# Kernel optimization log

Measured on AMD Instinct MI355X. Metric: run time of the kernel, lower is better.

## Reference

```python
import jax, jax.numpy as jnp
import numpy as np
from math import factorial, sqrt, pi

MUL = 8
LS = [0, 1, 2]                       # l values for both Rs_in and Rs_out
RS = [(MUL, l) for l in LS]
N_NODES = 20000
N_EDGES = 100000
FEAT = sum(m * (2 * l + 1) for m, l in RS)       # 72
R_TOT = sum(mo * mi * (2 * min(lo, li) + 1) for mo, lo in RS for mi, li in RS)  # 1216
L_MAX = max(LS) + max(LS)            # 4
RSH_DIM = (L_MAX + 1) ** 2           # 25
NB, H = 10, 100                      # radial basis size / hidden width
MIN_R, MAX_R = 0.7, 3.2
SWISH_SCALE = 1.679177               # e3nn rescaled swish factor


def _w3j_entry(j1, j2, j3, m1, m2, m3):
    # complex-basis Wigner 3j (Racah formula)
    if m1 + m2 + m3 != 0 or not (abs(j1 - j2) <= j3 <= j1 + j2):
        return 0.0
    t1, t2 = j2 - m1 - j3, j1 + m2 - j3
    kmin, kmax = max(0, t1, t2), min(j1 + j2 - j3, j1 - m1, j2 + m2)
    s = sum((-1) ** k / (factorial(k) * factorial(k - t1) * factorial(k - t2)
                         * factorial(j1 + j2 - j3 - k) * factorial(j1 - m1 - k) * factorial(j2 + m2 - k))
            for k in range(kmin, kmax + 1))
    pref = (-1) ** (j1 - j2 - m3) * sqrt(
        factorial(j1 + j2 - j3) * factorial(j1 - j2 + j3) * factorial(-j1 + j2 + j3) / factorial(j1 + j2 + j3 + 1)
        * factorial(j1 + m1) * factorial(j1 - m1) * factorial(j2 + m2) * factorial(j2 - m2)
        * factorial(j3 + m3) * factorial(j3 - m3))
    return pref * s


def _real_cob(l):
    # complex->real spherical-harmonic change of basis
    U = np.zeros((2 * l + 1, 2 * l + 1), dtype=complex)
    U[l, l] = 1.0
    s = 1.0 / np.sqrt(2.0)
    for m in range(1, l + 1):
        U[l + m, l + m] = (-1) ** m * s
        U[l + m, l - m] = s
        U[l - m, l - m] = 1j * s
        U[l - m, l + m] = -1j * ((-1) ** m) * s
    return U


def _wigner3j_real(l1, l2, l3):
    w = np.zeros((2 * l1 + 1, 2 * l2 + 1, 2 * l3 + 1))
    for m1 in range(-l1, l1 + 1):
        for m2 in range(-l2, l2 + 1):
            m3 = -m1 - m2
            if abs(m3) <= l3:
                w[m1 + l1, m2 + l2, m3 + l3] = _w3j_entry(l1, l2, l3, m1, m2, m3)
    T = np.einsum('am,bn,cp,mnp->abc', _real_cob(l1), _real_cob(l2), _real_cob(l3), w.astype(complex))
    C = T.real if np.linalg.norm(T.real) >= np.linalg.norm(T.imag) else T.imag
    n = np.linalg.norm(C)
    return (C / n if n > 0 else C).astype(np.float32)


# precomputed constants (coupling coefficients + normalization), as in MinimalNetwork.__init__
C3 = {(lo, li, lf): jnp.asarray(_wigner3j_real(lo, li, lf))
      for _, lo in RS for _, li in RS for lf in range(abs(lo - li), lo + li + 1)}


def _norm_coef():
    nc = np.zeros((len(RS), len(RS)), dtype=np.float32)
    for i, (_, lo) in enumerate(RS):
        num = sum(mi * (2 * min(lo, li) + 1) for mi, li in RS)
        nc[i, :] = sqrt(4 * pi) * sqrt(2 * lo + 1) / sqrt(num)
    return jnp.asarray(nc)

NORM = _norm_coef()


def _swish(x):
    return SWISH_SCALE * x * jax.nn.sigmoid(x)


def _radial(r, Ws):
    # GaussianRadialModel: gaussian basis -> 3 hidden swish layers -> linear out
    centers = jnp.linspace(MIN_R, MAX_R, NB)
    sigma = (MAX_R - MIN_R) / (NB - 1)
    x = jnp.exp(-(((r[:, None] - centers) / sigma) ** 2))
    for W in Ws[:-1]:
        x = _swish(x @ (W / jnp.sqrt(jnp.asarray(W.shape[0], x.dtype))))
    W = Ws[-1]
    return x @ (W / jnp.sqrt(jnp.asarray(W.shape[0], x.dtype)))


def _tensor_message(F_src, rsh, R):
    # F_src: [E, FEAT] gathered source features; rsh: [E, 25]; R: [E, R_TOT]
    E = F_src.shape[0]
    f_offs = np.cumsum([0] + [m * (2 * l + 1) for m, l in RS])
    msgs, r_off = [], 0
    for i, (U, lo) in enumerate(RS):
        acc = jnp.zeros((E, U, 2 * lo + 1), F_src.dtype)
        for j, (V, li) in enumerate(RS):
            nlf = 2 * min(lo, li) + 1
            Rb = R[:, r_off:r_off + U * V * nlf].reshape(E, U, V, nlf)
            r_off += U * V * nlf
            Fb = F_src[:, f_offs[j]:f_offs[j + 1]].reshape(E, V, 2 * li + 1)
            for fi, lf in enumerate(range(abs(lo - li), lo + li + 1)):
                # K[e,mo,mi] = sum_mf C3[mo,mi,mf] * Y_lf[e,mf]
                K = jnp.einsum('oif,ef->eoi', C3[(lo, li, lf)], rsh[:, lf * lf:(lf + 1) * (lf + 1)])
                acc = acc + NORM[i, j] * jnp.einsum('eoi,evi,euv->euo', K, Fb, Rb[..., fi])
        msgs.append(acc.reshape(E, -1))
    return jnp.concatenate(msgs, axis=-1)


def _forward(features, edge_index, radii, rsh, Ws):
    R = _radial(radii, Ws)                                     # [E, R_TOT]
    msg = _tensor_message(features[edge_index[0]], rsh, R)     # [E, FEAT]
    # scatter-add aggregation at target nodes (MessagePassing aggr='add')
    return jnp.zeros((features.shape[0], msg.shape[1]), msg.dtype).at[edge_index[1]].add(msg)


def setup_inputs() -> dict:
    key = jax.random.key(0)
    ks = jax.random.split(key, 8)
    features = jax.random.normal(ks[0], (N_NODES, FEAT), jnp.float32)
    edge_index = jax.random.randint(ks[1], (2, N_EDGES), 0, N_NODES)
    radii = MIN_R + (MAX_R - MIN_R) * jax.random.uniform(ks[2], (N_EDGES,), jnp.float32)
    rsh = jax.random.normal(ks[3], (N_EDGES, RSH_DIM), jnp.float32)
    W0 = jax.random.normal(ks[4], (NB, H), jnp.float32)
    W1 = jax.random.normal(ks[5], (H, H), jnp.float32)
    W2 = jax.random.normal(ks[6], (H, H), jnp.float32)
    W3 = jax.random.normal(ks[7], (H, R_TOT), jnp.float32)
    return {"features": features, "edge_index": edge_index, "radii": radii, "rsh": rsh,
            "W0": W0, "W1": W1, "W2": W2, "W3": W3}


def reference(features, edge_index, radii, rsh, W0, W1, W2, W3):
    return _forward(features, edge_index, radii, rsh, (W0, W1, W2, W3))
```

## Files before the change

kernel.cpp:

```cpp
#include <hip/hip_runtime.h>
#include <hip/hip_bf16.h>
#include <math.h>


#define FEATD 72
#define NCOL 1216
#define SWISH_SCALE 1.679177f

typedef __attribute__((ext_vector_type(8))) short bf16x8;
typedef __attribute__((ext_vector_type(4))) float f32x4;

constexpr int NCOMBO = 19;
constexpr int CB_LO[NCOMBO] = {0,0,0,1,1,1,1,1,1,1,2,2,2,2,2,2,2,2,2};
constexpr int CB_LI[NCOMBO] = {0,1,2,0,1,1,1,2,2,2,0,1,1,1,2,2,2,2,2};
constexpr int CB_LF[NCOMBO] = {0,1,2,1,0,1,2,1,2,3,2,1,2,3,0,1,2,3,4};
constexpr int CB_OFF[NCOMBO] = {0,1,10,35,44,53,80,125,170,245,350,375,420,495,600,625,700,825,1000};
constexpr int CB_SZ[NCOMBO]  = {1,9,25,9,9,27,45,45,75,105,25,45,75,105,25,75,125,175,225};
constexpr int C3TOT = 1225;

constexpr int C3OFFT[3][3][5] = {
  { {0,-1,-1,-1,-1}, {-1,1,-1,-1,-1}, {-1,-1,10,-1,-1} },
  { {-1,35,-1,-1,-1}, {44,53,80,-1,-1}, {-1,125,170,245,-1} },
  { {-1,-1,350,-1,-1}, {-1,375,420,495,-1}, {600,625,700,825,1000} }
};
constexpr int ROFFT[3][3] = {{0,64,128},{192,256,448},{640,704,896}};
constexpr int FOFFT[3]   = {0,8,32};

__device__ const double d_fact[11] = {1.,1.,2.,6.,24.,120.,720.,5040.,40320.,362880.,3628800.};

__device__ double w3j_entry(int j1,int j2,int j3,int m1,int m2,int m3){
  if (m1+m2+m3 != 0) return 0.0;
  int dj = j1-j2; if (dj<0) dj=-dj;
  if (j3 < dj || j3 > j1+j2) return 0.0;
  int t1 = j2 - m1 - j3, t2 = j1 + m2 - j3;
  int kmin = 0; if (t1>kmin) kmin=t1; if (t2>kmin) kmin=t2;
  int kmax = j1+j2-j3; if (j1-m1<kmax) kmax=j1-m1; if (j2+m2<kmax) kmax=j2+m2;
  double s = 0.0;
  for (int k=kmin;k<=kmax;++k){
    double den = d_fact[k]*d_fact[k-t1]*d_fact[k-t2]*d_fact[j1+j2-j3-k]
               * d_fact[j1-m1-k]*d_fact[j2+m2-k];
    s += ((k&1)? -1.0:1.0)/den;
  }
  double pref = sqrt(d_fact[j1+j2-j3]*d_fact[j1-j2+j3]*d_fact[-j1+j2+j3]/d_fact[j1+j2+j3+1]
               * d_fact[j1+m1]*d_fact[j1-m1]*d_fact[j2+m2]*d_fact[j2-m2]
               * d_fact[j3+m3]*d_fact[j3-m3]);
  int ex = j1-j2-m3;
  if (ex & 1) pref = -pref;
  return pref*s;
}

__device__ void cob(int l, int r, int c, double& re, double& im){
  re = 0.0; im = 0.0;
  int mr = r - l, mc = c - l;
  const double s = 0.70710678118654752440;
  if (mr == 0) { if (mc == 0) re = 1.0; return; }
  if (mr > 0) {
    if (mc == mr)       re = (mr & 1) ? -s : s;
    else if (mc == -mr) re = s;
  } else {
    int m = -mr;
    if (mc == -m)      im = s;
    else if (mc == m)  im = (m & 1) ? s : -s;
  }
}

__global__ void c3_combined_kernel(float* __restrict__ C3f){
  __shared__ double sre[225], sim[225];
  const int c = blockIdx.x;
  const int lo = CB_LO[c], li = CB_LI[c], lf = CB_LF[c];
  const int off = CB_OFF[c], sz = CB_SZ[c];
  const int n2 = 2*li+1, n3 = 2*lf+1;
  const int t = threadIdx.x;

  for (int p=t; p<sz; p+=64){
    int a = p/(n2*n3), b = (p/n3)%n2, g = p%n3;
    double re=0.0, im=0.0;
    for (int m1=-lo; m1<=lo; ++m1){
      for (int m2=-li; m2<=li; ++m2){
        int m3 = -m1-m2;
        if (m3 < -lf || m3 > lf) continue;
        double w = w3j_entry(lo,li,lf,m1,m2,m3);
        if (w == 0.0) continue;
        double r1,i1,r2,i2,r3,i3;
        cob(lo, a, m1+lo, r1,i1);
        cob(li, b, m2+li, r2,i2);
        cob(lf, g, m3+lf, r3,i3);
        double rr = r1*r2 - i1*i2, ri = r1*i2 + i1*r2;
        double fr = rr*r3 - ri*i3, fi = rr*i3 + ri*r3;
        re += fr*w; im += fi*w;
      }
    }
    sre[p] = re; sim[p] = im;
  }
  __syncthreads();
  double s2r=0.0, s2i=0.0;
  for (int p=t; p<sz; p+=64){ double x=sre[p], y=sim[p]; s2r+=x*x; s2i+=y*y; }
  for (int m=1; m<64; m<<=1){ s2r += __shfl_xor(s2r, m, 64); s2i += __shfl_xor(s2i, m, 64); }
  bool useRe = (s2r >= s2i);
  double n = sqrt(useRe ? s2r : s2i);
  double inv = (n > 0.0) ? 1.0/n : 1.0;
  for (int p=t; p<sz; p+=64){
    double v = useRe ? sre[p] : sim[p];
    C3f[off+p] = (float)(v*inv);
  }
}

__global__ __launch_bounds__(256) void prep_combined_kernel(
    const float* __restrict__ W3, const float* __restrict__ W1,
    const float* __restrict__ W2, __hip_bfloat16* __restrict__ W3t,
    __hip_bfloat16* __restrict__ W1t, __hip_bfloat16* __restrict__ W2t)
{
  int idx = blockIdx.x*256 + threadIdx.x;
  constexpr int NW3 = 1216*128;
  constexpr int HALF = 112*128;
  if (idx < NW3){
    int cp = idx >> 7, k = idx & 127;
    int chunk = cp >> 6, r = cp & 63;
    int lo = CB_LO[chunk], li = CB_LI[chunk], lf = CB_LF[chunk];
    int lmin = lo<li ? lo : li;
    int nlf = 2*lmin+1;
    int fi = lf - (lo>li ? lo-li : li-lo);
    int c = ROFFT[lo][li] + r*nlf + fi;
    float v = (k < 100) ? 0.1f*W3[(size_t)k*NCOL + c] : 0.f;
    int swz = (r*16 + (k>>3)) ^ (r&7);
    W3t[(size_t)chunk*8192 + swz*8 + (k&7)] = __float2bfloat16(v);
  } else if (idx < NW3 + 2*HALF){
    int r2 = idx - NW3;
    const float* W = (r2 < HALF) ? W1 : W2;
    __hip_bfloat16* Wt = (r2 < HALF) ? W1t : W2t;
    int r = (r2 < HALF) ? r2 : r2 - HALF;
    int o = r >> 7, k = r & 127;
    float v = (o < 100 && k < 100) ? 0.1f*W[k*100+o] : 0.f;
    int swz = (o*16 + (k>>3)) ^ (o&7);
    Wt[swz*8 + (k&7)] = __float2bfloat16(v);
  }
}

constexpr int OF_W   = 0;
constexpr int OF_RT  = 16384;
constexpr int OF_ACC = 33792;
constexpr int OF_F   = 44032;
constexpr int OF_KV  = 63488;
constexpr int OF_C3  = 76288;
constexpr int OF_SRC = 81188;
constexpr int OF_TGT = 81444;
constexpr int SMEM_SZ = 81700;

constexpr int OF_RW   = 0;
constexpr int OF_BAS  = 28672;
constexpr int OF_HA   = 31232;
constexpr int OF_HB   = 48640;

__device__ __forceinline__ float swishf(float s){
  return SWISH_SCALE * s / (1.f + __expf(-s));
}

__device__ __forceinline__ void stage_w(const __hip_bfloat16* __restrict__ Wt,
                                        char* sW, int t)
{
  const int lane = t & 63, wv = t >> 6;
  const char* g = (const char*)Wt;
  #pragma unroll
  for (int i=0; i<7; ++i){
    const char* gsrc = g + (i*256 + wv*64 + lane)*16;
    __builtin_amdgcn_global_load_lds(
        (const __attribute__((address_space(1))) unsigned int*)gsrc,
        (__attribute__((address_space(3))) unsigned int*)(sW + i*4096 + wv*1024),
        16, 0, 0);
  }
}

__device__ __forceinline__ void radial_layer_lds(
    const __hip_bfloat16* __restrict__ sIn,
    const char* __restrict__ sW,
    __hip_bfloat16* __restrict__ sOut,
    int wv, int lr, int lq)
{
  bf16x8 bf[4];
  #pragma unroll
  for (int ks=0; ks<4; ++ks)
    bf[ks] = *(const bf16x8*)&sIn[(wv*16+lr)*136 + ks*32 + lq*8];
  f32x4 acc[7] = {};
  #pragma unroll
  for (int ks=0; ks<4; ++ks)
    #pragma unroll
    for (int ot=0; ot<7; ++ot){
      const int row = ot*16 + lr;
      const int u = (row*16 + ks*4 + lq) ^ (row & 7);
      bf16x8 a = *(const bf16x8*)(sW + u*16);
      acc[ot] = __builtin_amdgcn_mfma_f32_16x16x32_bf16(a, bf[ks], acc[ot], 0, 0, 0);
    }
  #pragma unroll
  for (int ot=0; ot<7; ++ot){
    __hip_bfloat16 hv[4];
    #pragma unroll
    for (int r=0; r<4; ++r)
      hv[r] = __float2bfloat16(swishf(acc[ot][r]));
    *(short4*)&sOut[(wv*16+lr)*136 + ot*16 + lq*4] = *(short4*)hv;
  }
  {
    int lane = lq*16 + lr;
    int row = lane & 15, q = lane >> 4;
    short4 z = {0,0,0,0};
    *(short4*)&sOut[(wv*16+row)*136 + 112 + q*4] = z;
  }
}

__device__ __forceinline__ void stage_chunk(const __hip_bfloat16* __restrict__ W3t,
                                            int chunk, char* sW, int t)
{
  const int lane = t & 63, wv = t >> 6;
  const char* g = (const char*)W3t + (size_t)chunk*16384;
  #pragma unroll
  for (int r=0; r<4; ++r){
    const char* gsrc = g + (wv*256 + r*64 + lane)*16;
    __builtin_amdgcn_global_load_lds(
        (const __attribute__((address_space(1))) unsigned int*)gsrc,
        (__attribute__((address_space(3))) unsigned int*)(sW + wv*4096 + r*1024),
        16, 0, 0);
  }
}

template<int LO,int LI,int LF>
__device__ __forceinline__ void kv_sec(float* kvb, const float* sC3,
                                       const float* __restrict__ rshrow,
                                       int e, int role)
{
  constexpr int NO = 2*LO+1, NI = 2*LI+1, NF = 2*LF+1;
  constexpr int C3B = C3OFFT[LO][LI][LF];
  float y[NF];
  #pragma unroll
  for (int mf=0; mf<NF; ++mf) y[mf] = rshrow[LF*LF + mf];
  for (int it = role; it < NO*NI; it += 4){
    float s = 0.f;
    #pragma unroll
    for (int mf=0; mf<NF; ++mf) s += sC3[C3B + it*NF + mf] * y[mf];
    kvb[e*25 + it] = s;
  }
}

template<int LO,int LI>
__device__ __forceinline__ void consume_sec(
    const float* sRt, const float* sFf, const float* kvb, float* sAcc,
    int e, int role)
{
  constexpr int NO = 2*LO+1, NI = 2*LI+1;
  constexpr int FO = FOFFT[LI];
  float H[2][NI];
  #pragma unroll
  for (int du=0; du<2; ++du)
    #pragma unroll
    for (int mi=0; mi<NI; ++mi) H[du][mi] = 0.f;

  #pragma unroll
  for (int vg=0; vg<2; ++vg){
    float fb[4*NI];
    #pragma unroll
    for (int p=0; p<NI; ++p)
      *(f32x4*)&fb[p*4] = *(const f32x4*)&sFf[e*76 + FO + vg*4*NI + p*4];
    #pragma unroll
    for (int du=0; du<2; ++du){
      const int u = role*2 + du;
      f32x4 rv = *(const f32x4*)&sRt[e*68 + u*8 + vg*4];
      #pragma unroll
      for (int v=0; v<4; ++v)
        #pragma unroll
        for (int mi=0; mi<NI; ++mi)
          H[du][mi] += rv[v] * fb[v*NI + mi];
    }
  }
  const int u0 = role*2, u1 = role*2 + 1;
  const int b0 = e*40 + ((LO==0) ? u0 : (LO==1) ? u0*3 : u0*5);
  const int b1 = e*40 + ((LO==0) ? u1 : (LO==1) ? u1*3 : u1*5);
  #pragma unroll
  for (int o=0; o<NO; ++o){
    float s0 = 0.f, s1 = 0.f;
    #pragma unroll
    for (int mi=0; mi<NI; ++mi){
      float kvv = kvb[e*25 + o*NI + mi];
      s0 += kvv * H[0][mi];
      s1 += kvv * H[1][mi];
    }
    sAcc[b0 + o] += s0;
    sAcc[b1 + o] += s1;
  }
}

__device__ __forceinline__ void mfma_sec(const char* sW, float* sRt,
                                         const bf16x8 (&hf)[4],
                                         int wv, int lr, int lq)
{
  f32x4 a4[4] = {};
  #pragma unroll
  for (int ks=0; ks<4; ++ks){
    #pragma unroll
    for (int ct=0; ct<4; ++ct){
      const int row = ct*16 + lr;
      const int u   = (row*16 + (ks*4 + lq)) ^ (row & 7);
      bf16x8 a = *(const bf16x8*)(sW + u*16);
      a4[ct] = __builtin_amdgcn_mfma_f32_16x16x32_bf16(a, hf[ks], a4[ct], 0, 0, 0);
    }
  }
  #pragma unroll
  for (int ct=0; ct<4; ++ct)
    *(f32x4*)&sRt[(wv*16 + lr)*68 + ct*16 + lq*4] = a4[ct];
}

template<int J0,int W>
__device__ __forceinline__ void flush_group(float* sAcc, float* __restrict__ out,
                                            const int* sTgt, int eb, int t,
                                            float nrm, int E)
{
  const int lane = t & 63, wv = t >> 6;
  __builtin_amdgcn_wave_barrier();
  for (int p = lane; p < 16*W; p += 64){
    int el = wv*16 + p/W, j = p%W;
    if (eb + el < E)
      atomicAdd(&out[(size_t)sTgt[el]*FEATD + J0 + j], nrm * sAcc[el*40 + j]);
    sAcc[el*40 + j] = 0.f;
  }
  __builtin_amdgcn_wave_barrier();
}

template<int LO,int LI,int LF,int PLO,int PLI,int PFLUSH,int CUR>
__device__ __forceinline__ void phase_pl(
    int chunk, const __hip_bfloat16* __restrict__ W3t, const bf16x8 (&hf)[4],
    char* sW, float* sRt, float* sFf, float* sKV, const float* sC3,
    const float* __restrict__ rshrow, float* sAcc,
    float* __restrict__ out, const int* sTgt, int eb, int t, int E)
{
  const int e = t >> 2, role = t & 3;
  const int lane = t & 63, wv = t >> 6;
  const int lr = lane & 15, lq = lane >> 4;

  __syncthreads();
  stage_chunk(W3t, chunk, sW, t);

  kv_sec<LO,LI,LF>(sKV + CUR*1600, sC3, rshrow, e, role);
  if constexpr (PLO >= 0)
    consume_sec<PLO,PLI>(sRt, sFf, sKV + (1-CUR)*1600, sAcc, e, role);
  if constexpr (PFLUSH == 0)
    flush_group<0,8>(sAcc, out, sTgt, eb, t, 0.72360125f, E);
  if constexpr (PFLUSH == 1)
    flush_group<8,24>(sAcc, out, sTgt, eb, t, 0.8204867f, E);

  __syncthreads();
  mfma_sec(sW, sRt, hf, wv, lr, lq);
  __builtin_amdgcn_wave_barrier();
}

__global__ __launch_bounds__(256,2) void fused_kernel(
    const float* __restrict__ feats, const int* __restrict__ ei,
    const float* __restrict__ radii, const float* __restrict__ rsh,
    const float* __restrict__ W0,
    const __hip_bfloat16* __restrict__ W1t, const __hip_bfloat16* __restrict__ W2t,
    const __hip_bfloat16* __restrict__ W3t, const float* __restrict__ C3g,
    float* __restrict__ out, int E)
{
  __shared__ __align__(16) char smem[SMEM_SZ];
  char*  sW   = smem + OF_W;
  float* sRt  = (float*)(smem + OF_RT);
  float* sAcc = (float*)(smem + OF_ACC);
  float* sFf  = (float*)(smem + OF_F);
  float* sKV  = (float*)(smem + OF_KV);
  float* sC3  = (float*)(smem + OF_C3);
  int*   sSrc = (int*)(smem + OF_SRC);
  int*   sTgt = (int*)(smem + OF_TGT);
  char*  sWr  = smem + OF_RW;
  float* sbas = (float*)(smem + OF_BAS);
  __hip_bfloat16* hA = (__hip_bfloat16*)(smem + OF_HA);
  __hip_bfloat16* hB = (__hip_bfloat16*)(smem + OF_HB);

  const int t = threadIdx.x;
  const int eb = blockIdx.x*64;
  const int lane = t & 63, wv = t >> 6;
  const int lr = lane & 15, lq = lane >> 4;

  stage_w(W1t, sWr, t);

  for (int p=t; p<640; p+=256){
    int er = p/10, k = p%10;
    int eg = eb + er;
    float r = (eg < E) ? radii[eg] : 0.f;
    float c = 0.7f + (2.5f/9.0f)*(float)k;
    float d = (r - c) * (9.0f/2.5f);
    sbas[p] = __expf(-d*d);
  }
  __syncthreads();
  for (int p=t; p<6400; p+=256){
    int er = p/100, o = p%100;
    float s = 0.f;
    #pragma unroll
    for (int k=0;k<10;++k) s += sbas[er*10+k]*W0[k*100+o];
    hA[er*136+o] = __float2bfloat16(swishf(s*0.3162277660168379f));
  }
  for (int p=t; p<64*36; p+=256){
    int er = p/36, k = 100 + p%36;
    hA[er*136+k] = __float2bfloat16(0.f);
  }
  __syncthreads();

  radial_layer_lds(hA, sWr, hB, wv, lr, lq);
  __syncthreads();
  stage_w(W2t, sWr, t);
  __syncthreads();
  radial_layer_lds(hB, sWr, hA, wv, lr, lq);
  __builtin_amdgcn_wave_barrier();

  bf16x8 hf[4];
  #pragma unroll
  for (int ks=0; ks<4; ++ks)
    hf[ks] = *(const bf16x8*)&hA[(wv*16+lr)*136 + ks*32 + lq*8];

  __syncthreads();

  for (int p=t; p<2560; p+=256) sAcc[p] = 0.f;
  for (int p=t; p<64; p+=256){
    int e = eb + p;
    sSrc[p] = (e < E) ? ei[e] : 0;
    sTgt[p] = (e < E) ? ei[E + e] : 0;
  }
  for (int p=t; p<C3TOT; p+=256) sC3[p] = C3g[p];
  __syncthreads();
  for (int p=t; p<64*72; p+=256){
    int el = p/72, j = p%72;
    sFf[el*76 + j] = feats[(size_t)sSrc[el]*72 + j];
  }
  __syncthreads();

  int eg = eb + (t >> 2); if (eg > E-1) eg = E-1;
  const float* rshrow = rsh + (size_t)eg*25;

  phase_pl<0,0,0, -1,-1, -1, 0>( 0, W3t, hf, sW, sRt, sFf, sKV, sC3, rshrow, sAcc, out, sTgt, eb, t, E);
  phase_pl<0,1,1,  0, 0, -1, 1>( 1, W3t, hf, sW, sRt, sFf, sKV, sC3, rshrow, sAcc, out, sTgt, eb, t, E);
  phase_pl<0,2,2,  0, 1, -1, 0>( 2, W3t, hf, sW, sRt, sFf, sKV, sC3, rshrow, sAcc, out, sTgt, eb, t, E);
  phase_pl<1,0,1,  0, 2,  0, 1>( 3, W3t, hf, sW, sRt, sFf, sKV, sC3, rshrow, sAcc, out, sTgt, eb, t, E);
  phase_pl<1,1,0,  1, 0, -1, 0>( 4, W3t, hf, sW, sRt, sFf, sKV, sC3, rshrow, sAcc, out, sTgt, eb, t, E);
  phase_pl<1,1,1,  1, 1, -1, 1>( 5, W3t, hf, sW, sRt, sFf, sKV, sC3, rshrow, sAcc, out, sTgt, eb, t, E);
  phase_pl<1,1,2,  1, 1, -1, 0>( 6, W3t, hf, sW, sRt, sFf, sKV, sC3, rshrow, sAcc, out, sTgt, eb, t, E);
  phase_pl<1,2,1,  1, 1, -1, 1>( 7, W3t, hf, sW, sRt, sFf, sKV, sC3, rshrow, sAcc, out, sTgt, eb, t, E);
  phase_pl<1,2,2,  1, 2, -1, 0>( 8, W3t, hf, sW, sRt, sFf, sKV, sC3, rshrow, sAcc, out, sTgt, eb, t, E);
  phase_pl<1,2,3,  1, 2, -1, 1>( 9, W3t, hf, sW, sRt, sFf, sKV, sC3, rshrow, sAcc, out, sTgt, eb, t, E);
  phase_pl<2,0,2,  1, 2,  1, 0>(10, W3t, hf, sW, sRt, sFf, sKV, sC3, rshrow, sAcc, out, sTgt, eb, t, E);
  phase_pl<2,1,1,  2, 0, -1, 1>(11, W3t, hf, sW, sRt, sFf, sKV, sC3, rshrow, sAcc, out, sTgt, eb, t, E);
  phase_pl<2,1,2,  2, 1, -1, 0>(12, W3t, hf, sW, sRt, sFf, sKV, sC3, rshrow, sAcc, out, sTgt, eb, t, E);
  phase_pl<2,1,3,  2, 1, -1, 1>(13, W3t, hf, sW, sRt, sFf, sKV, sC3, rshrow, sAcc, out, sTgt, eb, t, E);
  phase_pl<2,2,0,  2, 1, -1, 0>(14, W3t, hf, sW, sRt, sFf, sKV, sC3, rshrow, sAcc, out, sTgt, eb, t, E);
  phase_pl<2,2,1,  2, 2, -1, 1>(15, W3t, hf, sW, sRt, sFf, sKV, sC3, rshrow, sAcc, out, sTgt, eb, t, E);
  phase_pl<2,2,2,  2, 2, -1, 0>(16, W3t, hf, sW, sRt, sFf, sKV, sC3, rshrow, sAcc, out, sTgt, eb, t, E);
  phase_pl<2,2,3,  2, 2, -1, 1>(17, W3t, hf, sW, sRt, sFf, sKV, sC3, rshrow, sAcc, out, sTgt, eb, t, E);
  phase_pl<2,2,4,  2, 2, -1, 0>(18, W3t, hf, sW, sRt, sFf, sKV, sC3, rshrow, sAcc, out, sTgt, eb, t, E);

  {
    const int e = t >> 2, role = t & 3;
    consume_sec<2,2>(sRt, sFf, sKV + 0*1600, sAcc, e, role);
    flush_group<32,40>(sAcc, out, sTgt, eb, t, 0.9341652f, E);
  }
}

extern "C" void kernel_launch(void* const* d_in, const int* in_sizes, int n_in,
                              void* d_out, int out_size, void* d_ws, size_t ws_size,
                              hipStream_t stream)
{
  const float* feats = (const float*)d_in[0];
  const int*   ei    = (const int*)d_in[1];
  const float* radii = (const float*)d_in[2];
  const float* rsh   = (const float*)d_in[3];
  const float* W0    = (const float*)d_in[4];
  const float* W1    = (const float*)d_in[5];
  const float* W2    = (const float*)d_in[6];
  const float* W3    = (const float*)d_in[7];
  float* out = (float*)d_out;
  const int E = in_sizes[2];

  const int EPAD = ((E + 63)/64)*64;
  const int NBLK = EPAD/64;

  char* ws = (char*)d_ws;
  size_t off_b = 0;
  float*  C3f = (float*)(ws + off_b);  off_b += 8192;
  __hip_bfloat16* W3t = (__hip_bfloat16*)(ws + off_b); off_b += 335872;
  __hip_bfloat16* W1t = (__hip_bfloat16*)(ws + off_b); off_b += 30720;
  __hip_bfloat16* W2t = (__hip_bfloat16*)(ws + off_b); off_b += 30720;

  hipMemsetAsync(out, 0, (size_t)out_size*sizeof(float), stream);

  c3_combined_kernel<<<dim3(NCOMBO), dim3(64), 0, stream>>>(C3f);
  prep_combined_kernel<<<dim3((1216*128 + 2*112*128 + 255)/256), dim3(256), 0, stream>>>(
      W3, W1, W2, W3t, W1t, W2t);

  fused_kernel<<<dim3(NBLK), dim3(256), 0, stream>>>(
      feats, ei, radii, rsh, W0, W1t, W2t, W3t, C3f, out, E);
}
```

Baseline: 340.8 us.

## Read MFMA weight fragments directly from global memory instead of staging in LDS

```diff
diff --git a/kernel.cpp b/kernel.cpp
--- a/kernel.cpp
+++ b/kernel.cpp
@@ -111,70 +111,56 @@
     __hip_bfloat16* __restrict__ W1t, __hip_bfloat16* __restrict__ W2t)
 {
   int idx = blockIdx.x*256 + threadIdx.x;
-  constexpr int NW3 = 1216*128;
-  constexpr int HALF = 112*128;
+  constexpr int NW3 = 19*8192;
+  constexpr int HALF = 7*4*64*8;
   if (idx < NW3){
-    int cp = idx >> 7, k = idx & 127;
-    int chunk = cp >> 6, r = cp & 63;
+    int j = idx & 7, lane = (idx>>3)&63, kc = (idx>>9)&15, chunk = idx>>13;
+    int ks = kc & 3, ct = kc >> 2;
+    int r = ct*16 + (lane&15);
+    int k = ks*32 + (lane>>4)*8 + j;
     int lo = CB_LO[chunk], li = CB_LI[chunk], lf = CB_LF[chunk];
     int lmin = lo<li ? lo : li;
     int nlf = 2*lmin+1;
     int fi = lf - (lo>li ? lo-li : li-lo);
     int c = ROFFT[lo][li] + r*nlf + fi;
     float v = (k < 100) ? 0.1f*W3[(size_t)k*NCOL + c] : 0.f;
-    int swz = (r*16 + (k>>3)) ^ (r&7);
-    W3t[(size_t)chunk*8192 + swz*8 + (k&7)] = __float2bfloat16(v);
+    W3t[idx] = __float2bfloat16(v);
   } else if (idx < NW3 + 2*HALF){
     int r2 = idx - NW3;
     const float* W = (r2 < HALF) ? W1 : W2;
     __hip_bfloat16* Wt = (r2 < HALF) ? W1t : W2t;
     int r = (r2 < HALF) ? r2 : r2 - HALF;
-    int o = r >> 7, k = r & 127;
+    int j = r & 7, lane = (r>>3)&63, kc = r>>9;
+    int ks = kc & 3, ot = kc >> 2;
+    int o = ot*16 + (lane&15);
+    int k = ks*32 + (lane>>4)*8 + j;
     float v = (o < 100 && k < 100) ? 0.1f*W[k*100+o] : 0.f;
-    int swz = (o*16 + (k>>3)) ^ (o&7);
-    Wt[swz*8 + (k&7)] = __float2bfloat16(v);
-  }
-}
-
-constexpr int OF_W   = 0;
-constexpr int OF_RT  = 16384;
-constexpr int OF_ACC = 33792;
-constexpr int OF_F   = 44032;
-constexpr int OF_KV  = 63488;
-constexpr int OF_C3  = 76288;
-constexpr int OF_SRC = 81188;
-constexpr int OF_TGT = 81444;
-constexpr int SMEM_SZ = 81700;
-
-constexpr int OF_RW   = 0;
-constexpr int OF_BAS  = 28672;
-constexpr int OF_HA   = 31232;
-constexpr int OF_HB   = 48640;
+    Wt[r] = __float2bfloat16(v);
+  }
+}
+
+constexpr int OF_RT  = 0;
+constexpr int OF_ACC = 17408;
+constexpr int OF_F   = 27648;
+constexpr int OF_KV  = 47104;
+constexpr int OF_C3  = 53504;
+constexpr int OF_SRC = 58404;
+constexpr int OF_TGT = 58660;
+constexpr int SMEM_SZ = 58916;
+
+constexpr int OF_BAS  = 0;
+constexpr int OF_HA   = 2560;
+constexpr int OF_HB   = 19968;
 
 __device__ __forceinline__ float swishf(float s){
   return SWISH_SCALE * s / (1.f + __expf(-s));
 }
 
-__device__ __forceinline__ void stage_w(const __hip_bfloat16* __restrict__ Wt,
-                                        char* sW, int t)
-{
-  const int lane = t & 63, wv = t >> 6;
-  const char* g = (const char*)Wt;
-  #pragma unroll
-  for (int i=0; i<7; ++i){
-    const char* gsrc = g + (i*256 + wv*64 + lane)*16;
-    __builtin_amdgcn_global_load_lds(
-        (const __attribute__((address_space(1))) unsigned int*)gsrc,
-        (__attribute__((address_space(3))) unsigned int*)(sW + i*4096 + wv*1024),
-        16, 0, 0);
-  }
-}
-
-__device__ __forceinline__ void radial_layer_lds(
+__device__ __forceinline__ void radial_layer_glb(
     const __hip_bfloat16* __restrict__ sIn,
-    const char* __restrict__ sW,
+    const __hip_bfloat16* __restrict__ Wt,
     __hip_bfloat16* __restrict__ sOut,
-    int wv, int lr, int lq)
+    int lane, int wv, int lr, int lq)
 {
   bf16x8 bf[4];
   #pragma unroll
@@ -185,9 +171,7 @@
   for (int ks=0; ks<4; ++ks)
     #pragma unroll
     for (int ot=0; ot<7; ++ot){
-      const int row = ot*16 + lr;
-      const int u = (row*16 + ks*4 + lq) ^ (row & 7);
-      bf16x8 a = *(const bf16x8*)(sW + u*16);
+      bf16x8 a = *(const bf16x8*)&Wt[((ot*4+ks)*64 + lane)*8];
       acc[ot] = __builtin_amdgcn_mfma_f32_16x16x32_bf16(a, bf[ks], acc[ot], 0, 0, 0);
     }
   #pragma unroll
@@ -199,25 +183,10 @@
     *(short4*)&sOut[(wv*16+lr)*136 + ot*16 + lq*4] = *(short4*)hv;
   }
   {
-    int lane = lq*16 + lr;
-    int row = lane & 15, q = lane >> 4;
+    int l2 = lq*16 + lr;
+    int row = l2 & 15, q = l2 >> 4;
     short4 z = {0,0,0,0};
     *(short4*)&sOut[(wv*16+row)*136 + 112 + q*4] = z;
-  }
-}
-
-__device__ __forceinline__ void stage_chunk(const __hip_bfloat16* __restrict__ W3t,
-                                            int chunk, char* sW, int t)
-{
-  const int lane = t & 63, wv = t >> 6;
-  const char* g = (const char*)W3t + (size_t)chunk*16384;
-  #pragma unroll
-  for (int r=0; r<4; ++r){
-    const char* gsrc = g + (wv*256 + r*64 + lane)*16;
-    __builtin_amdgcn_global_load_lds(
-        (const __attribute__((address_space(1))) unsigned int*)gsrc,
-        (__attribute__((address_space(3))) unsigned int*)(sW + wv*4096 + r*1024),
-        16, 0, 0);
   }
 }
 
@@ -286,18 +255,17 @@
   }
 }
 
-__device__ __forceinline__ void mfma_sec(const char* sW, float* sRt,
-                                         const bf16x8 (&hf)[4],
-                                         int wv, int lr, int lq)
+__device__ __forceinline__ void mfma_sec_glb(
+    const __hip_bfloat16* __restrict__ gW,
+    float* sRt, const bf16x8 (&hf)[4],
+    int lane, int wv, int lr, int lq)
 {
   f32x4 a4[4] = {};
   #pragma unroll
   for (int ks=0; ks<4; ++ks){
     #pragma unroll
     for (int ct=0; ct<4; ++ct){
-      const int row = ct*16 + lr;
-      const int u   = (row*16 + (ks*4 + lq)) ^ (row & 7);
-      bf16x8 a = *(const bf16x8*)(sW + u*16);
+      bf16x8 a = *(const bf16x8*)&gW[((ct*4+ks)*64 + lane)*8];
       a4[ct] = __builtin_amdgcn_mfma_f32_16x16x32_bf16(a, hf[ks], a4[ct], 0, 0, 0);
     }
   }
@@ -322,30 +290,20 @@
   __builtin_amdgcn_wave_barrier();
 }
 
-template<int LO,int LI,int LF,int PLO,int PLI,int PFLUSH,int CUR>
-__device__ __forceinline__ void phase_pl(
+template<int LO,int LI,int LF>
+__device__ __forceinline__ void phase(
     int chunk, const __hip_bfloat16* __restrict__ W3t, const bf16x8 (&hf)[4],
-    char* sW, float* sRt, float* sFf, float* sKV, const float* sC3,
-    const float* __restrict__ rshrow, float* sAcc,
-    float* __restrict__ out, const int* sTgt, int eb, int t, int E)
+    float* sRt, float* sFf, float* sKV, const float* sC3,
+    const float* __restrict__ rshrow, float* sAcc, int t)
 {
   const int e = t >> 2, role = t & 3;
   const int lane = t & 63, wv = t >> 6;
   const int lr = lane & 15, lq = lane >> 4;
 
-  __syncthreads();
-  stage_chunk(W3t, chunk, sW, t);
-
-  kv_sec<LO,LI,LF>(sKV + CUR*1600, sC3, rshrow, e, role);
-  if constexpr (PLO >= 0)
-    consume_sec<PLO,PLI>(sRt, sFf, sKV + (1-CUR)*1600, sAcc, e, role);
-  if constexpr (PFLUSH == 0)
-    flush_group<0,8>(sAcc, out, sTgt, eb, t, 0.72360125f, E);
-  if constexpr (PFLUSH == 1)
-    flush_group<8,24>(sAcc, out, sTgt, eb, t, 0.8204867f, E);
-
-  __syncthreads();
-  mfma_sec(sW, sRt, hf, wv, lr, lq);
+  kv_sec<LO,LI,LF>(sKV, sC3, rshrow, e, role);
+  mfma_sec_glb(W3t + (size_t)chunk*8192, sRt, hf, lane, wv, lr, lq);
+  __builtin_amdgcn_wave_barrier();
+  consume_sec<LO,LI>(sRt, sFf, sKV, sAcc, e, role);
   __builtin_amdgcn_wave_barrier();
 }
 
@@ -358,7 +316,6 @@
     float* __restrict__ out, int E)
 {
   __shared__ __align__(16) char smem[SMEM_SZ];
-  char*  sW   = smem + OF_W;
   float* sRt  = (float*)(smem + OF_RT);
   float* sAcc = (float*)(smem + OF_ACC);
   float* sFf  = (float*)(smem + OF_F);
@@ -366,7 +323,6 @@
   float* sC3  = (float*)(smem + OF_C3);
   int*   sSrc = (int*)(smem + OF_SRC);
   int*   sTgt = (int*)(smem + OF_TGT);
-  char*  sWr  = smem + OF_RW;
   float* sbas = (float*)(smem + OF_BAS);
   __hip_bfloat16* hA = (__hip_bfloat16*)(smem + OF_HA);
   __hip_bfloat16* hB = (__hip_bfloat16*)(smem + OF_HB);
@@ -375,8 +331,6 @@
   const int eb = blockIdx.x*64;
   const int lane = t & 63, wv = t >> 6;
   const int lr = lane & 15, lq = lane >> 4;
-
-  stage_w(W1t, sWr, t);
 
   for (int p=t; p<640; p+=256){
     int er = p/10, k = p%10;
@@ -400,11 +354,9 @@
   }
   __syncthreads();
 
-  radial_layer_lds(hA, sWr, hB, wv, lr, lq);
-  __syncthreads();
-  stage_w(W2t, sWr, t);
-  __syncthreads();
-  radial_layer_lds(hB, sWr, hA, wv, lr, lq);
+  radial_layer_glb(hA, W1t, hB, lane, wv, lr, lq);
+  __builtin_amdgcn_wave_barrier();
+  radial_layer_glb(hB, W2t, hA, lane, wv, lr, lq);
   __builtin_amdgcn_wave_barrier();
 
   bf16x8 hf[4];
@@ -431,31 +383,30 @@
   int eg = eb + (t >> 2); if (eg > E-1) eg = E-1;
   const float* rshrow = rsh + (size_t)eg*25;
 
-  phase_pl<0,0,0, -1,-1, -1, 0>( 0, W3t, hf, sW, sRt, sFf, sKV, sC3, rshrow, sAcc, out, sTgt, eb, t, E);
-  phase_pl<0,1,1,  0, 0, -1, 1>( 1, W3t, hf, sW, sRt, sFf, sKV, sC3, rshrow, sAcc, out, sTgt, eb, t, E);
-  phase_pl<0,2,2,  0, 1, -1, 0>( 2, W3t, hf, sW, sRt, sFf, sKV, sC3, rshrow, sAcc, out, sTgt, eb, t, E);
-  phase_pl<1,0,1,  0, 2,  0, 1>( 3, W3t, hf, sW, sRt, sFf, sKV, sC3, rshrow, sAcc, out, sTgt, eb, t, E);
-  phase_pl<1,1,0,  1, 0, -1, 0>( 4, W3t, hf, sW, sRt, sFf, sKV, sC3, rshrow, sAcc, out, sTgt, eb, t, E);
-  phase_pl<1,1,1,  1, 1, -1, 1>( 5, W3t, hf, sW, sRt, sFf, sKV, sC3, rshrow, sAcc, out, sTgt, eb, t, E);
-  phase_pl<1,1,2,  1, 1, -1, 0>( 6, W3t, hf, sW, sRt, sFf, sKV, sC3, rshrow, sAcc, out, sTgt, eb, t, E);
-  phase_pl<1,2,1,  1, 1, -1, 1>( 7, W3t, hf, sW, sRt, sFf, sKV, sC3, rshrow, sAcc, out, sTgt, eb, t, E);
-  phase_pl<1,2,2,  1, 2, -1, 0>( 8, W3t, hf, sW, sRt, sFf, sKV, sC3, rshrow, sAcc, out, sTgt, eb, t, E);
-  phase_pl<1,2,3,  1, 2, -1, 1>( 9, W3t, hf, sW, sRt, sFf, sKV, sC3, rshrow, sAcc, out, sTgt, eb, t, E);
-  phase_pl<2,0,2,  1, 2,  1, 0>(10, W3t, hf, sW, sRt, sFf, sKV, sC3, rshrow, sAcc, out, sTgt, eb, t, E);
-  phase_pl<2,1,1,  2, 0, -1, 1>(11, W3t, hf, sW, sRt, sFf, sKV, sC3, rshrow, sAcc, out, sTgt, eb, t, E);
-  phase_pl<2,1,2,  2, 1, -1, 0>(12, W3t, hf, sW, sRt, sFf, sKV, sC3, rshrow, sAcc, out, sTgt, eb, t, E);
-  phase_pl<2,1,3,  2, 1, -1, 1>(13, W3t, hf, sW, sRt, sFf, sKV, sC3, rshrow, sAcc, out, sTgt, eb, t, E);
-  phase_pl<2,2,0,  2, 1, -1, 0>(14, W3t, hf, sW, sRt, sFf, sKV, sC3, rshrow, sAcc, out, sTgt, eb, t, E);
-  phase_pl<2,2,1,  2, 2, -1, 1>(15, W3t, hf, sW, sRt, sFf, sKV, sC3, rshrow, sAcc, out, sTgt, eb, t, E);
-  phase_pl<2,2,2,  2, 2, -1, 0>(16, W3t, hf, sW, sRt, sFf, sKV, sC3, rshrow, sAcc, out, sTgt, eb, t, E);
-  phase_pl<2,2,3,  2, 2, -1, 1>(17, W3t, hf, sW, sRt, sFf, sKV, sC3, rshrow, sAcc, out, sTgt, eb, t, E);
-  phase_pl<2,2,4,  2, 2, -1, 0>(18, W3t, hf, sW, sRt, sFf, sKV, sC3, rshrow, sAcc, out, sTgt, eb, t, E);
-
-  {
-    const int e = t >> 2, role = t & 3;
-    consume_sec<2,2>(sRt, sFf, sKV + 0*1600, sAcc, e, role);
-    flush_group<32,40>(sAcc, out, sTgt, eb, t, 0.9341652f, E);
-  }
+  phase<0,0,0>( 0, W3t, hf, sRt, sFf, sKV, sC3, rshrow, sAcc, t);
+  phase<0,1,1>( 1, W3t, hf, sRt, sFf, sKV, sC3, rshrow, sAcc, t);
+  phase<0,2,2>( 2, W3t, hf, sRt, sFf, sKV, sC3, rshrow, sAcc, t);
+  flush_group<0,8>(sAcc, out, sTgt, eb, t, 0.72360125f, E);
+
+  phase<1,0,1>( 3, W3t, hf, sRt, sFf, sKV, sC3, rshrow, sAcc, t);
+  phase<1,1,0>( 4, W3t, hf, sRt, sFf, sKV, sC3, rshrow, sAcc, t);
+  phase<1,1,1>( 5, W3t, hf, sRt, sFf, sKV, sC3, rshrow, sAcc, t);
+  phase<1,1,2>( 6, W3t, hf, sRt, sFf, sKV, sC3, rshrow, sAcc, t);
+  phase<1,2,1>( 7, W3t, hf, sRt, sFf, sKV, sC3, rshrow, sAcc, t);
+  phase<1,2,2>( 8, W3t, hf, sRt, sFf, sKV, sC3, rshrow, sAcc, t);
+  phase<1,2,3>( 9, W3t, hf, sRt, sFf, sKV, sC3, rshrow, sAcc, t);
+  flush_group<8,24>(sAcc, out, sTgt, eb, t, 0.8204867f, E);
+
+  phase<2,0,2>(10, W3t, hf, sRt, sFf, sKV, sC3, rshrow, sAcc, t);
+  phase<2,1,1>(11, W3t, hf, sRt, sFf, sKV, sC3, rshrow, sAcc, t);
+  phase<2,1,2>(12, W3t, hf, sRt, sFf, sKV, sC3, rshrow, sAcc, t);
+  phase<2,1,3>(13, W3t, hf, sRt, sFf, sKV, sC3, rshrow, sAcc, t);
+  phase<2,2,0>(14, W3t, hf, sRt, sFf, sKV, sC3, rshrow, sAcc, t);
+  phase<2,2,1>(15, W3t, hf, sRt, sFf, sKV, sC3, rshrow, sAcc, t);
+  phase<2,2,2>(16, W3t, hf, sRt, sFf, sKV, sC3, rshrow, sAcc, t);
+  phase<2,2,3>(17, W3t, hf, sRt, sFf, sKV, sC3, rshrow, sAcc, t);
+  phase<2,2,4>(18, W3t, hf, sRt, sFf, sKV, sC3, rshrow, sAcc, t);
+  flush_group<32,40>(sAcc, out, sTgt, eb, t, 0.9341652f, E);
 }
 
 extern "C" void kernel_launch(void* const* d_in, const int* in_sizes, int n_in,
@@ -486,7 +437,7 @@
   hipMemsetAsync(out, 0, (size_t)out_size*sizeof(float), stream);
 
   c3_combined_kernel<<<dim3(NCOMBO), dim3(64), 0, stream>>>(C3f);
-  prep_combined_kernel<<<dim3((1216*128 + 2*112*128 + 255)/256), dim3(256), 0, stream>>>(
+  prep_combined_kernel<<<dim3((19*8192 + 2*14336 + 255)/256), dim3(256), 0, stream>>>(
       W3, W1, W2, W3t, W1t, W2t);
 
   fused_kernel<<<dim3(NBLK), dim3(256), 0, stream>>>(
```

Result: no change. 347.1 us (+1.8%).
